# Kernel tuning notes

Measured on AMD Instinct MI355X. Metric: run time of the kernel, lower is better.

Reference implementation:

```python
import jax, jax.numpy as jnp
import numpy as np

B, T, IN_DIM, OUT_DIM = 1024, 64, 8, 2
H, K, HIDDEN = 3, 5, 256
LOG_STD_MIN, LOG_STD_MAX = -20.0, 2.0


def setup_inputs() -> dict:
    key = jax.random.key(0)
    ks = jax.random.split(key, 12)
    def lin(k, fan_in, fan_out):
        b = 1.0 / np.sqrt(fan_in)
        return jax.random.uniform(k, (fan_in, fan_out), jnp.float32, -b, b)
    inp = {
        'state': jax.random.normal(ks[0], (B, T, IN_DIM), jnp.float32),
        'noise': jax.random.normal(ks[1], (B, T, OUT_DIM), jnp.float32),
        'Wq': lin(ks[2], IN_DIM, K * H),
        'Wk': lin(ks[3], K, K * H),
        'Wv': lin(ks[4], K, K * H),
        'W1': lin(ks[5], K * H + IN_DIM, HIDDEN),
        'b1': jnp.zeros((HIDDEN,), jnp.float32),
        'W2': lin(ks[6], HIDDEN, HIDDEN),
        'b2': jnp.zeros((HIDDEN,), jnp.float32),
        'Wmu': jax.random.uniform(ks[7], (HIDDEN, OUT_DIM), jnp.float32, -0.003, 0.003),
        'bmu': jax.random.uniform(ks[8], (OUT_DIM,), jnp.float32, -0.003, 0.003),
        'Wls': jax.random.uniform(ks[9], (HIDDEN, OUT_DIM), jnp.float32, -0.003, 0.003),
        'bls': jax.random.uniform(ks[10], (OUT_DIM,), jnp.float32, -0.003, 0.003),
    }
    return inp


# static off-diagonal neighbor indices: row i -> all j != i
_OFFDIAG = np.array([[j for j in range(T) if j != i] for i in range(T)], dtype=np.int32)


def _forward(state, noise, Wq, Wk, Wv, W1, b1, W2, b2, Wmu, bmu, Wls, bls):
    b, t, _ = state.shape
    # rel[b,i,j] = state[b,j,:4] - state[b,i,:4]
    rel4 = state[:, None, :, 0:4] - state[:, :, None, 0:4]          # [b,t,t,4] (x,y,vx,vy)
    x_comp = rel4[..., 0::2]                                         # [x, vx]
    y_comp = rel4[..., 1::2]                                         # [y, vy]
    ang = (-state[:, :, 7] + 0.5 * jnp.pi)[:, None, :, None]         # varies with j (own-ref of key agent)
    c, s = jnp.cos(ang), jnp.sin(ang)
    xn = x_comp * c - y_comp * s                                     # [x', vx']
    yn = x_comp * s + y_comp * c                                     # [y', vy']
    rel = jnp.stack([xn[..., 0], yn[..., 0], xn[..., 1], yn[..., 1]], axis=-1)  # [b,t,t,4]
    # drop self-pairs (diagonal) -> [b,t,t-1,4]
    idx = jnp.asarray(_OFFDIAG)
    rel_od = rel[:, jnp.arange(t)[:, None], idx]
    r = jnp.sqrt(rel_od[..., 0] ** 2 + rel_od[..., 1] ** 2)[..., None]   # [b,t,t-1,1]
    r_trans = jax.nn.sigmoid(1.0 - 5.0 * (r - 0.2))                       # 1/(1+exp(-1+5(r-0.2)))
    rel_n = jnp.concatenate([rel_od[..., 0:2] / r, rel_od[..., 2:4], r_trans], axis=-1)  # [b,t,t-1,5]
    h, k = H, K
    q = (state @ Wq).reshape(b, t, h, k)                              # [b,t,h,k]
    keys = (rel_n @ Wk).reshape(b, t, t - 1, h, k)                    # [b,t,n,h,k]
    vals = (rel_n @ Wv).reshape(b, t, t - 1, h, k)
    scores = jnp.einsum('btnhk,bthk->bthn', keys, q) / jnp.sqrt(jnp.float32(k))
    w = jax.nn.softmax(scores, axis=-1)                               # over t-1 neighbors
    att = jnp.einsum('bthn,btnhk->bthk', w, vals).reshape(b, t, h * k)
    x = jnp.concatenate([att, state], axis=-1)
    x = jax.nn.relu(x @ W1 + b1)
    x = jax.nn.relu(x @ W2 + b2)
    mu = jnp.tanh(x @ Wmu + bmu)
    log_std = jnp.tanh(x @ Wls + bls)
    log_std = LOG_STD_MIN + 0.5 * (LOG_STD_MAX - LOG_STD_MIN) * (log_std + 1.0)
    std = jnp.exp(log_std)
    z = mu + std * noise                                              # rsample with explicit noise
    action = jnp.tanh(z)
    # Normal(mu,std).log_prob(z) with (z-mu)/std == noise
    log_prob = -0.5 * noise ** 2 - log_std - 0.5 * jnp.log(2.0 * jnp.pi)
    log_prob = log_prob - jnp.log(1.0 - action ** 2 + 1e-7)
    log_prob = jnp.sum(log_prob, axis=-1, keepdims=True)
    return action, log_prob


def reference(state, noise, Wq, Wk, Wv, W1, b1, W2, b2, Wmu, bmu, Wls, bls):
    return _forward(state, noise, Wq, Wk, Wv, W1, b1, W2, b2, Wmu, bmu, Wls, bls)
```

## Files before the change

kernel.cpp:

```cpp
#include <hip/hip_runtime.h>
#include <math.h>

#define NROWS 65536

typedef short bf16x8 __attribute__((ext_vector_type(8)));
typedef float f32x4  __attribute__((ext_vector_type(4)));

__device__ __forceinline__ unsigned short f2bf(float x){
    unsigned int u = __float_as_uint(x);
    u += 0x7FFFu + ((u >> 16) & 1u);
    return (unsigned short)(u >> 16);
}

template<int CTRL, int RM>
__device__ __forceinline__ float dpp_add(float v){
    int m = __builtin_amdgcn_update_dpp(0, __float_as_int(v), CTRL, RM, 0xF, 1);
    return v + __int_as_float(m);
}
__device__ __forceinline__ float rowsum16(float v){
    v = dpp_add<0x111, 0xF>(v);
    v = dpp_add<0x112, 0xF>(v);
    v = dpp_add<0x114, 0xF>(v);
    v = dpp_add<0x118, 0xF>(v);
    return v;
}

__global__ __launch_bounds__(256) void prep_kernel(
    const float* __restrict__ W2, const float* __restrict__ W1,
    unsigned short* __restrict__ w2frag, unsigned short* __restrict__ w1frag)
{
    const int bx = blockIdx.x, t = threadIdx.x;
    if (bx < 128){
        const int ct = bx >> 3, kk = bx & 7;
        #pragma unroll
        for (int s = 0; s < 2; ++s){
            int f = t * 2 + s;
            int lane = f >> 3, e = f & 7;
            int k = kk * 32 + (lane >> 4) * 8 + e;
            int c = ct * 16 + (lane & 15);
            w2frag[(size_t)(ct * 8 + kk) * 512 + f] = f2bf(W2[k * 256 + c]);
        }
    } else {
        #pragma unroll
        for (int s = 0; s < 32; ++s){
            int flat = t * 32 + s;
            int ct = flat >> 9, r = flat & 511;
            int lane = r >> 3, e = r & 7;
            int k = (lane >> 4) * 8 + e;
            int c = ct * 16 + (lane & 15);
            w1frag[flat] = (k < 23) ? f2bf(W1[k * 256 + c]) : (unsigned short)0;
        }
    }
}

__global__ __launch_bounds__(512, 4) void actor_kernel(
    const float* __restrict__ state, const float* __restrict__ noise,
    const float* __restrict__ Wq, const float* __restrict__ Wk,
    const float* __restrict__ Wv,
    const unsigned short* __restrict__ w1frag, const float* __restrict__ b1,
    const unsigned short* __restrict__ w2frag, const float* __restrict__ b2,
    const float* __restrict__ Wmu, const float* __restrict__ bmu,
    const float* __restrict__ Wls, const float* __restrict__ bls,
    float* __restrict__ action_out, float* __restrict__ logprob_out)
{
    __shared__ float sLDS[64 * 9];
    __shared__ float pjLDS[64 * 8];
    __shared__ float qkLDS[64 * 17];
    __shared__ __align__(16) unsigned short x0LDS[64 * 40];
    __shared__ float headLDS[8 * 64 * 5];
    __shared__ __align__(16) unsigned char uni[8 * 64 * 25 * 4];
    float* mergeLDS = (float*)uni;
    unsigned short* h1LDS = (unsigned short*)uni;

    const int t    = threadIdx.x;
    const int lane = t & 63;
    const int w    = t >> 6;
    const int lm   = lane & 15;
    const int lq   = lane >> 4;
    const int b    = blockIdx.x;

    {
        float v = state[(size_t)b * 512 + t];
        int r = t >> 3, c = t & 7;
        sLDS[r * 9 + c] = v;
        if (c < 4) pjLDS[r * 8 + c] = v;
    }
    __syncthreads();

    if (t < 192){
        const int row = t & 63, h = t >> 6;
        float s[8];
        #pragma unroll
        for (int d = 0; d < 8; ++d) s[d] = sLDS[row * 9 + d];
        float q[5];
        #pragma unroll
        for (int e = 0; e < 5; ++e){
            int m = h * 5 + e;
            float acc = 0.f;
            #pragma unroll
            for (int d = 0; d < 8; ++d) acc += s[d] * Wq[d * 15 + m];
            q[e] = acc;
        }
        #pragma unroll
        for (int f = 0; f < 5; ++f){
            float acc = 0.f;
            #pragma unroll
            for (int kk = 0; kk < 5; ++kk) acc += Wk[f * 15 + h * 5 + kk] * q[kk];
            qkLDS[row * 17 + h * 5 + f] = acc * 0.64519834f;
        }
    } else if (w == 7){
        const int row = lane;
        float ang = 1.5707963267948966f - sLDS[row * 9 + 7];
        float sn, cs;
        __sincosf(ang, &sn, &cs);
        pjLDS[row * 8 + 4] = sn;
        pjLDS[row * 8 + 5] = cs;
    }
    __syncthreads();

    {
        const int i = lane;
        float si0 = sLDS[i * 9 + 0], si1 = sLDS[i * 9 + 1];
        float si2 = sLDS[i * 9 + 2], si3 = sLDS[i * 9 + 3];
        float qkv[15];
        #pragma unroll
        for (int m = 0; m < 15; ++m) qkv[m] = qkLDS[i * 17 + m];

        float mh[2][3], sh[2][3], g[2][3][5];
        #pragma unroll
        for (int st = 0; st < 2; ++st)
            #pragma unroll
            for (int h = 0; h < 3; ++h){
                mh[st][h] = -1e30f; sh[st][h] = 0.f;
                #pragma unroll
                for (int f = 0; f < 5; ++f) g[st][h][f] = 0.f;
            }

        #pragma unroll
        for (int jj = 0; jj < 4; ++jj){
            #pragma unroll
            for (int st = 0; st < 2; ++st){
                const int j = (w << 3) + jj * 2 + st;
                float4 pj = *(const float4*)&pjLDS[j * 8];
                float sn = pjLDS[j * 8 + 4], cs = pjLDS[j * 8 + 5];
                float d0 = pj.x - si0, d1 = pj.y - si1, d2 = pj.z - si2, d3 = pj.w - si3;
                float xn0 = d0 * cs - d1 * sn, yn0 = d0 * sn + d1 * cs;
                float xn1 = d2 * cs - d3 * sn, yn1 = d2 * sn + d3 * cs;
                float r2v = xn0 * xn0 + yn0 * yn0;
                bool self = (j == i);
                float inv_r = self ? 0.f : rsqrtf(r2v);
                float rv = r2v * inv_r;
                float ex = exp2f(rv * 7.2134752f - 2.8853901f);
                float f4 = 1.f / (1.f + ex);
                float f0 = xn0 * inv_r, f1 = yn0 * inv_r;
                #pragma unroll
                for (int h = 0; h < 3; ++h){
                    float sc = f0 * qkv[h*5] + f1 * qkv[h*5+1] + xn1 * qkv[h*5+2]
                             + yn1 * qkv[h*5+3] + f4 * qkv[h*5+4];
                    sc = self ? -1e30f : sc;
                    float mn = fmaxf(mh[st][h], sc);
                    float e  = exp2f(sc - mn);
                    float sca = exp2f(mh[st][h] - mn);
                    mh[st][h] = mn;
                    sh[st][h] = sh[st][h] * sca + e;
                    g[st][h][0] = g[st][h][0] * sca + e * f0;
                    g[st][h][1] = g[st][h][1] * sca + e * f1;
                    g[st][h][2] = g[st][h][2] * sca + e * xn1;
                    g[st][h][3] = g[st][h][3] * sca + e * yn1;
                    g[st][h][4] = g[st][h][4] * sca + e * f4;
                }
            }
        }
        #pragma unroll
        for (int h = 0; h < 3; ++h){
            float M = fmaxf(mh[0][h], mh[1][h]);
            float sA = exp2f(mh[0][h] - M), sB = exp2f(mh[1][h] - M);
            float* mp = &mergeLDS[(w * 64 + i) * 25 + h * 8];
            mp[0] = M;
            mp[1] = sh[0][h] * sA + sh[1][h] * sB;
            #pragma unroll
            for (int f = 0; f < 5; ++f) mp[2 + f] = g[0][h][f] * sA + g[1][h][f] * sB;
        }
    }
    __syncthreads();

    if (t < 192){
        const int i = t & 63, h = t >> 6;
        float M = -1e30f;
        float pm[8], ps[8], pg[8][5];
        #pragma unroll
        for (int ww = 0; ww < 8; ++ww){
            const float* mp = &mergeLDS[(ww * 64 + i) * 25 + h * 8];
            pm[ww] = mp[0]; ps[ww] = mp[1];
            #pragma unroll
            for (int f = 0; f < 5; ++f) pg[ww][f] = mp[2 + f];
            M = fmaxf(M, pm[ww]);
        }
        float stot = 0.f, gt[5] = {0.f, 0.f, 0.f, 0.f, 0.f};
        #pragma unroll
        for (int ww = 0; ww < 8; ++ww){
            float sca = exp2f(pm[ww] - M);
            stot += ps[ww] * sca;
            #pragma unroll
            for (int f = 0; f < 5; ++f) gt[f] += pg[ww][f] * sca;
        }
        float inv = 1.f / stot;
        #pragma unroll
        for (int f = 0; f < 5; ++f) gt[f] *= inv;
        #pragma unroll
        for (int of = 0; of < 5; ++of){
            int m = h * 5 + of;
            float av = gt[0] * Wv[m] + gt[1] * Wv[15 + m] + gt[2] * Wv[30 + m]
                     + gt[3] * Wv[45 + m] + gt[4] * Wv[60 + m];
            x0LDS[i * 40 + m] = f2bf(av);
        }
    } else if (w == 3){
        const int i = lane;
        #pragma unroll
        for (int d = 0; d < 8; ++d) x0LDS[i * 40 + 15 + d] = f2bf(sLDS[i * 9 + d]);
        #pragma unroll
        for (int e = 23; e < 32; ++e) x0LDS[i * 40 + e] = 0;
    }
    __syncthreads();

    {
        bf16x8 afr[4];
        #pragma unroll
        for (int rt = 0; rt < 4; ++rt)
            afr[rt] = *(const bf16x8*)&x0LDS[(rt * 16 + lm) * 40 + lq * 8];
        #pragma unroll
        for (int ci = 0; ci < 2; ++ci){
            const int ct = w * 2 + ci;
            bf16x8 bfr = *(const bf16x8*)&w1frag[(size_t)ct * 512 + lane * 8];
            float bb = b1[ct * 16 + lm];
            #pragma unroll
            for (int rt = 0; rt < 4; ++rt){
                f32x4 c0 = {0.f, 0.f, 0.f, 0.f};
                c0 = __builtin_amdgcn_mfma_f32_16x16x32_bf16(afr[rt], bfr, c0, 0, 0, 0);
                #pragma unroll
                for (int p = 0; p < 4; ++p)
                    h1LDS[(rt * 16 + lq * 4 + p) * 264 + ct * 16 + lm] = f2bf(fmaxf(c0[p] + bb, 0.f));
            }
        }
    }
    __syncthreads();

    {
        f32x4 acc[4][2];
        #pragma unroll
        for (int rt = 0; rt < 4; ++rt)
            #pragma unroll
            for (int ci = 0; ci < 2; ++ci) acc[rt][ci] = (f32x4){0.f, 0.f, 0.f, 0.f};

        #pragma unroll
        for (int kk = 0; kk < 8; ++kk){
            bf16x8 arf[4], brf[2];
            #pragma unroll
            for (int rt = 0; rt < 4; ++rt)
                arf[rt] = *(const bf16x8*)&h1LDS[(rt * 16 + lm) * 264 + kk * 32 + lq * 8];
            #pragma unroll
            for (int ci = 0; ci < 2; ++ci)
                brf[ci] = *(const bf16x8*)&w2frag[(size_t)((w * 2 + ci) * 8 + kk) * 512 + lane * 8];
            #pragma unroll
            for (int rt = 0; rt < 4; ++rt)
                #pragma unroll
                for (int ci = 0; ci < 2; ++ci)
                    acc[rt][ci] = __builtin_amdgcn_mfma_f32_16x16x32_bf16(arf[rt], brf[ci], acc[rt][ci], 0, 0, 0);
        }

        float bb[2];
        float2 wm[2], wl[2];
        #pragma unroll
        for (int ci = 0; ci < 2; ++ci){
            int c = (w * 2 + ci) * 16 + lm;
            bb[ci] = b2[c];
            wm[ci] = *(const float2*)&Wmu[c * 2];
            wl[ci] = *(const float2*)&Wls[c * 2];
        }
        #pragma unroll
        for (int rt = 0; rt < 4; ++rt){
            #pragma unroll
            for (int p = 0; p < 4; ++p){
                float m0 = 0.f, m1 = 0.f, l0 = 0.f, l1 = 0.f;
                #pragma unroll
                for (int ci = 0; ci < 2; ++ci){
                    float hv = fmaxf(acc[rt][ci][p] + bb[ci], 0.f);
                    m0 += hv * wm[ci].x;
                    m1 += hv * wm[ci].y;
                    l0 += hv * wl[ci].x;
                    l1 += hv * wl[ci].y;
                }
                m0 = rowsum16(m0); m1 = rowsum16(m1);
                l0 = rowsum16(l0); l1 = rowsum16(l1);
                if (lm == 15){
                    int row = rt * 16 + lq * 4 + p;
                    float* hp = &headLDS[(w * 64 + row) * 5];
                    hp[0] = m0; hp[1] = m1; hp[2] = l0; hp[3] = l1;
                }
            }
        }
    }
    __syncthreads();

    if (t < 64){
        const int row = t;
        float m0 = 0.f, m1 = 0.f, l0 = 0.f, l1 = 0.f;
        #pragma unroll
        for (int ww = 0; ww < 8; ++ww){
            const float* hp = &headLDS[(ww * 64 + row) * 5];
            m0 += hp[0]; m1 += hp[1]; l0 += hp[2]; l1 += hp[3];
        }
        const size_t grow = (size_t)b * 64 + row;
        float n0 = noise[grow * 2 + 0];
        float n1 = noise[grow * 2 + 1];
        float lp = 0.f;
        {
            float mu = tanhf(m0 + bmu[0]);
            float ls = tanhf(l0 + bls[0]);
            ls = -20.f + 11.f * (ls + 1.f);
            float sd = expf(ls);
            float a = tanhf(mu + sd * n0);
            action_out[grow * 2 + 0] = a;
            lp += -0.5f * n0 * n0 - ls - 0.9189385332046727f - logf(1.f - a * a + 1e-7f);
        }
        {
            float mu = tanhf(m1 + bmu[1]);
            float ls = tanhf(l1 + bls[1]);
            ls = -20.f + 11.f * (ls + 1.f);
            float sd = expf(ls);
            float a = tanhf(mu + sd * n1);
            action_out[grow * 2 + 1] = a;
            lp += -0.5f * n1 * n1 - ls - 0.9189385332046727f - logf(1.f - a * a + 1e-7f);
        }
        logprob_out[grow] = lp;
    }
}

extern "C" void kernel_launch(void* const* d_in, const int* in_sizes, int n_in,
                              void* d_out, int out_size, void* d_ws, size_t ws_size,
                              hipStream_t stream)
{
    (void)in_sizes; (void)n_in; (void)out_size; (void)ws_size;
    const float* state = (const float*)d_in[0];
    const float* noise = (const float*)d_in[1];
    const float* Wq  = (const float*)d_in[2];
    const float* Wk  = (const float*)d_in[3];
    const float* Wv  = (const float*)d_in[4];
    const float* W1  = (const float*)d_in[5];
    const float* b1  = (const float*)d_in[6];
    const float* W2  = (const float*)d_in[7];
    const float* b2  = (const float*)d_in[8];
    const float* Wmu = (const float*)d_in[9];
    const float* bmu = (const float*)d_in[10];
    const float* Wls = (const float*)d_in[11];
    const float* bls = (const float*)d_in[12];

    unsigned short* w2frag = (unsigned short*)d_ws;
    unsigned short* w1frag = w2frag + 65536;

    float* action_out  = (float*)d_out;
    float* logprob_out = (float*)d_out + (size_t)NROWS * 2;

    prep_kernel<<<129, 256, 0, stream>>>(W2, W1, w2frag, w1frag);
    actor_kernel<<<1024, 512, 0, stream>>>(state, noise, Wq, Wk, Wv,
        w1frag, b1, w2frag, b2, Wmu, bmu, Wls, bls, action_out, logprob_out);
}
```

Before: 126.3 us.

## Repartition attention so 8 lanes share a row with DPP reductions and two-pass softmax

Attention is now split so each query row is handled by 8 lanes of one wave, each covering 8 neighbours. Partial sums are combined with DPP butterfly reductions instead of per-wave partials merged through shared memory. The online softmax is replaced by two passes (max, then exp-sum), which recomputes the geometric features but drops the rescale exponentials, one barrier and the 192-thread merge stage. Shared memory shrinks by aliasing buffers, and launch bounds are raised to 6 waves per SIMD, which may force register spills.

```diff
diff --git a/kernel.cpp b/kernel.cpp
--- a/kernel.cpp
+++ b/kernel.cpp
@@ -22,6 +22,23 @@
     v = dpp_add<0x112, 0xF>(v);
     v = dpp_add<0x114, 0xF>(v);
     v = dpp_add<0x118, 0xF>(v);
+    return v;
+}
+__device__ __forceinline__ float bfly8_add(float v){
+    v = dpp_add<0xB1, 0xF>(v);
+    v = dpp_add<0x4E, 0xF>(v);
+    v = dpp_add<0x141, 0xF>(v);
+    return v;
+}
+template<int CTRL>
+__device__ __forceinline__ float dpp_max1(float v){
+    int m = __builtin_amdgcn_update_dpp(__float_as_int(v), __float_as_int(v), CTRL, 0xF, 0xF, 0);
+    return fmaxf(v, __int_as_float(m));
+}
+__device__ __forceinline__ float bfly8_max(float v){
+    v = dpp_max1<0xB1>(v);
+    v = dpp_max1<0x4E>(v);
+    v = dpp_max1<0x141>(v);
     return v;
 }
 
@@ -53,7 +70,7 @@
     }
 }
 
-__global__ __launch_bounds__(512, 4) void actor_kernel(
+__global__ __launch_bounds__(512, 6) void actor_kernel(
     const float* __restrict__ state, const float* __restrict__ noise,
     const float* __restrict__ Wq, const float* __restrict__ Wk,
     const float* __restrict__ Wv,
@@ -63,14 +80,13 @@
     const float* __restrict__ Wls, const float* __restrict__ bls,
     float* __restrict__ action_out, float* __restrict__ logprob_out)
 {
-    __shared__ float sLDS[64 * 9];
-    __shared__ float pjLDS[64 * 8];
-    __shared__ float qkLDS[64 * 17];
+    __shared__ __align__(16) unsigned char uniA[64 * 264 * 2];
+    float* sLDS  = (float*)uniA;
+    float* pjLDS = sLDS + 576;
+    float* qkLDS = pjLDS + 512;
+    unsigned short* h1LDS = (unsigned short*)uniA;
     __shared__ __align__(16) unsigned short x0LDS[64 * 40];
     __shared__ float headLDS[8 * 64 * 5];
-    __shared__ __align__(16) unsigned char uni[8 * 64 * 25 * 4];
-    float* mergeLDS = (float*)uni;
-    unsigned short* h1LDS = (unsigned short*)uni;
 
     const int t    = threadIdx.x;
     const int lane = t & 63;
@@ -119,107 +135,95 @@
     __syncthreads();
 
     {
-        const int i = lane;
-        float si0 = sLDS[i * 9 + 0], si1 = sLDS[i * 9 + 1];
-        float si2 = sLDS[i * 9 + 2], si3 = sLDS[i * 9 + 3];
+        const int il = lane >> 3;
+        const int js = lane & 7;
+        const int i  = w * 8 + il;
+        const float si0 = sLDS[i * 9 + 0], si1 = sLDS[i * 9 + 1];
+        const float si2 = sLDS[i * 9 + 2], si3 = sLDS[i * 9 + 3];
         float qkv[15];
         #pragma unroll
         for (int m = 0; m < 15; ++m) qkv[m] = qkLDS[i * 17 + m];
 
-        float mh[2][3], sh[2][3], g[2][3][5];
-        #pragma unroll
-        for (int st = 0; st < 2; ++st)
-            #pragma unroll
-            for (int h = 0; h < 3; ++h){
-                mh[st][h] = -1e30f; sh[st][h] = 0.f;
-                #pragma unroll
-                for (int f = 0; f < 5; ++f) g[st][h][f] = 0.f;
+        float M0 = -1e30f, M1 = -1e30f, M2 = -1e30f;
+        #pragma unroll
+        for (int jj = 0; jj < 8; ++jj){
+            const int j = jj * 8 + js;
+            float4 pj = *(const float4*)&pjLDS[j * 8];
+            float sn = pjLDS[j * 8 + 4], cs = pjLDS[j * 8 + 5];
+            float d0 = pj.x - si0, d1 = pj.y - si1, d2 = pj.z - si2, d3 = pj.w - si3;
+            float xn0 = d0 * cs - d1 * sn, yn0 = d0 * sn + d1 * cs;
+            float xn1 = d2 * cs - d3 * sn, yn1 = d2 * sn + d3 * cs;
+            float r2v = xn0 * xn0 + yn0 * yn0;
+            bool self = (j == i);
+            float inv_r = self ? 0.f : rsqrtf(r2v);
+            float rv = r2v * inv_r;
+            float ex = exp2f(rv * 7.2134752f - 2.8853901f);
+            float f4 = 1.f / (1.f + ex);
+            float f0 = xn0 * inv_r, f1 = yn0 * inv_r;
+            float sc0 = f0*qkv[0]  + f1*qkv[1]  + xn1*qkv[2]  + yn1*qkv[3]  + f4*qkv[4];
+            float sc1 = f0*qkv[5]  + f1*qkv[6]  + xn1*qkv[7]  + yn1*qkv[8]  + f4*qkv[9];
+            float sc2 = f0*qkv[10] + f1*qkv[11] + xn1*qkv[12] + yn1*qkv[13] + f4*qkv[14];
+            M0 = fmaxf(M0, self ? -1e30f : sc0);
+            M1 = fmaxf(M1, self ? -1e30f : sc1);
+            M2 = fmaxf(M2, self ? -1e30f : sc2);
+        }
+        M0 = bfly8_max(M0); M1 = bfly8_max(M1); M2 = bfly8_max(M2);
+
+        float s0 = 0.f, s1 = 0.f, s2 = 0.f;
+        float g0[5] = {0,0,0,0,0}, g1[5] = {0,0,0,0,0}, g2[5] = {0,0,0,0,0};
+        #pragma unroll
+        for (int jj = 0; jj < 8; ++jj){
+            const int j = jj * 8 + js;
+            float4 pj = *(const float4*)&pjLDS[j * 8];
+            float sn = pjLDS[j * 8 + 4], cs = pjLDS[j * 8 + 5];
+            float d0 = pj.x - si0, d1 = pj.y - si1, d2 = pj.z - si2, d3 = pj.w - si3;
+            float xn0 = d0 * cs - d1 * sn, yn0 = d0 * sn + d1 * cs;
+            float xn1 = d2 * cs - d3 * sn, yn1 = d2 * sn + d3 * cs;
+            float r2v = xn0 * xn0 + yn0 * yn0;
+            bool self = (j == i);
+            float inv_r = self ? 0.f : rsqrtf(r2v);
+            float rv = r2v * inv_r;
+            float ex = exp2f(rv * 7.2134752f - 2.8853901f);
+            float f4 = 1.f / (1.f + ex);
+            float f0 = xn0 * inv_r, f1 = yn0 * inv_r;
+            float sc0 = f0*qkv[0]  + f1*qkv[1]  + xn1*qkv[2]  + yn1*qkv[3]  + f4*qkv[4];
+            float sc1 = f0*qkv[5]  + f1*qkv[6]  + xn1*qkv[7]  + yn1*qkv[8]  + f4*qkv[9];
+            float sc2 = f0*qkv[10] + f1*qkv[11] + xn1*qkv[12] + yn1*qkv[13] + f4*qkv[14];
+            float e0 = self ? 0.f : exp2f(sc0 - M0);
+            float e1 = self ? 0.f : exp2f(sc1 - M1);
+            float e2 = self ? 0.f : exp2f(sc2 - M2);
+            s0 += e0; s1 += e1; s2 += e2;
+            g0[0] += e0*f0; g0[1] += e0*f1; g0[2] += e0*xn1; g0[3] += e0*yn1; g0[4] += e0*f4;
+            g1[0] += e1*f0; g1[1] += e1*f1; g1[2] += e1*xn1; g1[3] += e1*yn1; g1[4] += e1*f4;
+            g2[0] += e2*f0; g2[1] += e2*f1; g2[2] += e2*xn1; g2[3] += e2*yn1; g2[4] += e2*f4;
+        }
+        s0 = bfly8_add(s0); s1 = bfly8_add(s1); s2 = bfly8_add(s2);
+        #pragma unroll
+        for (int f = 0; f < 5; ++f){
+            g0[f] = bfly8_add(g0[f]);
+            g1[f] = bfly8_add(g1[f]);
+            g2[f] = bfly8_add(g2[f]);
+        }
+        float i0 = 1.f / s0, i1 = 1.f / s1, i2 = 1.f / s2;
+
+        #pragma unroll
+        for (int mm = 0; mm < 2; ++mm){
+            int m = js * 2 + mm;
+            if (m < 15){
+                float G0 = (m < 5) ? g0[0] : (m < 10) ? g1[0] : g2[0];
+                float G1 = (m < 5) ? g0[1] : (m < 10) ? g1[1] : g2[1];
+                float G2 = (m < 5) ? g0[2] : (m < 10) ? g1[2] : g2[2];
+                float G3 = (m < 5) ? g0[3] : (m < 10) ? g1[3] : g2[3];
+                float G4 = (m < 5) ? g0[4] : (m < 10) ? g1[4] : g2[4];
+                float I  = (m < 5) ? i0    : (m < 10) ? i1    : i2;
+                float av = (G0 * Wv[m] + G1 * Wv[15 + m] + G2 * Wv[30 + m]
+                          + G3 * Wv[45 + m] + G4 * Wv[60 + m]) * I;
+                x0LDS[i * 40 + m] = f2bf(av);
             }
-
-        #pragma unroll
-        for (int jj = 0; jj < 4; ++jj){
-            #pragma unroll
-            for (int st = 0; st < 2; ++st){
-                const int j = (w << 3) + jj * 2 + st;
-                float4 pj = *(const float4*)&pjLDS[j * 8];
-                float sn = pjLDS[j * 8 + 4], cs = pjLDS[j * 8 + 5];
-                float d0 = pj.x - si0, d1 = pj.y - si1, d2 = pj.z - si2, d3 = pj.w - si3;
-                float xn0 = d0 * cs - d1 * sn, yn0 = d0 * sn + d1 * cs;
-                float xn1 = d2 * cs - d3 * sn, yn1 = d2 * sn + d3 * cs;
-                float r2v = xn0 * xn0 + yn0 * yn0;
-                bool self = (j == i);
-                float inv_r = self ? 0.f : rsqrtf(r2v);
-                float rv = r2v * inv_r;
-                float ex = exp2f(rv * 7.2134752f - 2.8853901f);
-                float f4 = 1.f / (1.f + ex);
-                float f0 = xn0 * inv_r, f1 = yn0 * inv_r;
-                #pragma unroll
-                for (int h = 0; h < 3; ++h){
-                    float sc = f0 * qkv[h*5] + f1 * qkv[h*5+1] + xn1 * qkv[h*5+2]
-                             + yn1 * qkv[h*5+3] + f4 * qkv[h*5+4];
-                    sc = self ? -1e30f : sc;
-                    float mn = fmaxf(mh[st][h], sc);
-                    float e  = exp2f(sc - mn);
-                    float sca = exp2f(mh[st][h] - mn);
-                    mh[st][h] = mn;
-                    sh[st][h] = sh[st][h] * sca + e;
-                    g[st][h][0] = g[st][h][0] * sca + e * f0;
-                    g[st][h][1] = g[st][h][1] * sca + e * f1;
-                    g[st][h][2] = g[st][h][2] * sca + e * xn1;
-                    g[st][h][3] = g[st][h][3] * sca + e * yn1;
-                    g[st][h][4] = g[st][h][4] * sca + e * f4;
-                }
-            }
-        }
-        #pragma unroll
-        for (int h = 0; h < 3; ++h){
-            float M = fmaxf(mh[0][h], mh[1][h]);
-            float sA = exp2f(mh[0][h] - M), sB = exp2f(mh[1][h] - M);
-            float* mp = &mergeLDS[(w * 64 + i) * 25 + h * 8];
-            mp[0] = M;
-            mp[1] = sh[0][h] * sA + sh[1][h] * sB;
-            #pragma unroll
-            for (int f = 0; f < 5; ++f) mp[2 + f] = g[0][h][f] * sA + g[1][h][f] * sB;
-        }
-    }
-    __syncthreads();
-
-    if (t < 192){
-        const int i = t & 63, h = t >> 6;
-        float M = -1e30f;
-        float pm[8], ps[8], pg[8][5];
-        #pragma unroll
-        for (int ww = 0; ww < 8; ++ww){
-            const float* mp = &mergeLDS[(ww * 64 + i) * 25 + h * 8];
-            pm[ww] = mp[0]; ps[ww] = mp[1];
-            #pragma unroll
-            for (int f = 0; f < 5; ++f) pg[ww][f] = mp[2 + f];
-            M = fmaxf(M, pm[ww]);
-        }
-        float stot = 0.f, gt[5] = {0.f, 0.f, 0.f, 0.f, 0.f};
-        #pragma unroll
-        for (int ww = 0; ww < 8; ++ww){
-            float sca = exp2f(pm[ww] - M);
-            stot += ps[ww] * sca;
-            #pragma unroll
-            for (int f = 0; f < 5; ++f) gt[f] += pg[ww][f] * sca;
-        }
-        float inv = 1.f / stot;
-        #pragma unroll
-        for (int f = 0; f < 5; ++f) gt[f] *= inv;
-        #pragma unroll
-        for (int of = 0; of < 5; ++of){
-            int m = h * 5 + of;
-            float av = gt[0] * Wv[m] + gt[1] * Wv[15 + m] + gt[2] * Wv[30 + m]
-                     + gt[3] * Wv[45 + m] + gt[4] * Wv[60 + m];
-            x0LDS[i * 40 + m] = f2bf(av);
-        }
-    } else if (w == 3){
-        const int i = lane;
-        #pragma unroll
-        for (int d = 0; d < 8; ++d) x0LDS[i * 40 + 15 + d] = f2bf(sLDS[i * 9 + d]);
-        #pragma unroll
-        for (int e = 23; e < 32; ++e) x0LDS[i * 40 + e] = 0;
+        }
+        x0LDS[i * 40 + 15 + js] = f2bf(sLDS[i * 9 + js]);
+        x0LDS[i * 40 + 23 + js] = 0;
+        if (js == 0) x0LDS[i * 40 + 31] = 0;
     }
     __syncthreads();
 
```

Result: slower. 212.3 us (+68.1%).
